# Optimization experiments

Hardware: AMD Instinct MI355X
Metric: run time of the kernel (lower is better)

## Reference

```python
import jax, jax.numpy as jnp
import numpy as np
from functools import partial

B, S, D = 64, 1024, 1024
C = 10  # number of chained GRU steps (self.c)


def setup_inputs() -> dict:
    key = jax.random.key(0)
    ks = jax.random.split(key, 8)
    sc = 1.0 / np.sqrt(D)
    return {
        "feat": jax.random.normal(ks[0], (B, S, D), dtype=jnp.float32),
        "a_w": jax.random.normal(ks[1], (D,), dtype=jnp.float32) * sc,          # Linear(D,1,bias=False)
        "W_ih": jax.random.normal(ks[2], (3 * D, D + 1), dtype=jnp.float32) * sc,  # GRU input weights (r,z,n)
        "W_hh": jax.random.normal(ks[3], (3 * D, D), dtype=jnp.float32) * sc,      # GRU hidden weights (r,z,n)
        "b_ih": jax.random.normal(ks[4], (3 * D,), dtype=jnp.float32) * sc,
        "b_hh": jax.random.normal(ks[5], (3 * D,), dtype=jnp.float32) * sc,
        "W_out": jax.random.normal(ks[6], (1, D), dtype=jnp.float32) * sc,         # out_layer Linear(D,1)
        "b_out": jax.random.normal(ks[7], (1,), dtype=jnp.float32) * sc,
    }


def reference(feat, a_w, W_ih, W_hh, b_ih, b_hh, W_out, b_out):
    # Attention pooling: softmax over sequence dim of a scalar score per frame.
    logits = jnp.einsum("bsd,d->bs", feat, a_w)                 # [B, S]
    w = jax.nn.softmax(logits, axis=1)                           # [B, S]
    pooled = jnp.einsum("bs,bsd->bd", w, feat)                  # [B, D]

    def gru_step(carry, _):
        h, score = carry
        x = jnp.concatenate([pooled, score], axis=-1)            # [B, D+1]
        gi = x @ W_ih.T + b_ih                                   # [B, 3D]
        gh = h @ W_hh.T + b_hh                                   # [B, 3D]
        i_r, i_z, i_n = jnp.split(gi, 3, axis=-1)
        h_r, h_z, h_n = jnp.split(gh, 3, axis=-1)
        r = jax.nn.sigmoid(i_r + h_r)
        z = jax.nn.sigmoid(i_z + h_z)
        n = jnp.tanh(i_n + r * h_n)
        h_new = (1.0 - z) * n + z * h
        score_new = jax.nn.sigmoid(h_new @ W_out.T + b_out)      # [B, 1]
        return (h_new, score_new), score_new

    h0 = jnp.zeros_like(pooled)                                  # GRU hidden starts at zero
    s0 = jnp.zeros((pooled.shape[0], 1), dtype=pooled.dtype)     # zero_score initial chain input
    _, scores = jax.lax.scan(gru_step, (h0, s0), None, length=C)  # scores: [C, B, 1]
    out = jnp.transpose(scores[..., 0], (1, 0))                  # [B, C]
    return out
```

## Files before the change

kernel.cpp:

```cpp
#include <hip/hip_runtime.h>
#include <hip/hip_bf16.h>
#include <math.h>

#define B 64
#define S 1024
#define D 1024
#define C 10
#define TD 3072

typedef __attribute__((ext_vector_type(8))) short s8v;
typedef __attribute__((ext_vector_type(4))) float f4v;
typedef unsigned long long u64;

__device__ __forceinline__ float wave_sum_bc(float v) {
    #pragma unroll
    for (int off = 1; off < 64; off <<= 1) v += __shfl_xor(v, off, 64);
    return v;
}
__device__ __forceinline__ float sigm(float x) { return 1.0f / (1.0f + expf(-x)); }
__device__ __forceinline__ short f2bf(float f) {
    __hip_bfloat16 h = __float2bfloat16(f);
    return *reinterpret_cast<short*>(&h);
}
__device__ __forceinline__ u64 aload64(u64* p) {
    return __hip_atomic_load(p, __ATOMIC_RELAXED, __HIP_MEMORY_SCOPE_AGENT);
}
__device__ __forceinline__ void astore64(u64* p, u64 v) {
    __hip_atomic_store(p, v, __ATOMIC_RELAXED, __HIP_MEMORY_SCOPE_AGENT);
}
__device__ __forceinline__ float aloadf(float* p) {
    return __hip_atomic_load(p, __ATOMIC_RELAXED, __HIP_MEMORY_SCOPE_AGENT);
}
__device__ __forceinline__ void astoref(float* p, float v) {
    __hip_atomic_store(p, v, __ATOMIC_RELAXED, __HIP_MEMORY_SCOPE_AGENT);
}

__global__ __launch_bounds__(256) void k_pre(const float* __restrict__ feat,
        const float* __restrict__ a_w, const float* __restrict__ W_ih,
        const float* __restrict__ W_hh, float* __restrict__ part, float* __restrict__ ml,
        short* __restrict__ BihP, short* __restrict__ BhhP, float* __restrict__ wscore,
        unsigned* __restrict__ bar) {
    __shared__ float sacc[4][1024];
    __shared__ float sml[4][2];
    int n = blockIdx.x, tid = threadIdx.x;

    if (n >= 1024) {
        if (n < 4096) {
            int rel = n - 1024;
            const float* Wsrc = (rel < 1536) ? W_ih : W_hh;
            short* dst = (rel < 1536) ? BihP : BhhP;
            int stride = (rel < 1536) ? (D + 1) : D;
            int rn = (rel < 1536) ? rel : rel - 1536;
            int gid = rn * 256 + tid;
            int fid = gid >> 6, l = gid & 63;
            int s = fid & 31, g = (fid >> 5) % 3, dt = fid / 96;
            int row = g * 1024 + dt * 16 + (l & 15);
            int k0 = s * 32 + ((l >> 4) << 3);
            const float* src = Wsrc + (size_t)row * stride + k0;
            short v[8];
            #pragma unroll
            for (int j = 0; j < 8; ++j) v[j] = f2bf(src[j]);
            short* d = dst + ((size_t)fid * 64 + l) * 8;
            #pragma unroll
            for (int j = 0; j < 8; ++j) d[j] = v[j];
        } else {
            int j = (n - 4096) * 256 + tid;
            wscore[j] = W_ih[(size_t)j * (D + 1) + D];
            if (n == 4096 && tid < 64) bar[tid] = 0u;
        }
        return;
    }

    int ch = n & 15, b = n >> 4;
    int w = tid >> 6, lane = tid & 63;
    float4 aw[4], acc[4];
    #pragma unroll
    for (int r = 0; r < 4; ++r) {
        aw[r] = *reinterpret_cast<const float4*>(&a_w[r * 256 + lane * 4]);
        acc[r] = make_float4(0.f, 0.f, 0.f, 0.f);
    }
    float m = -INFINITY, l = 0.f;
    const float* fb = feat + ((size_t)b * S + ch * 64 + w * 16) * D;
    for (int i = 0; i < 16; ++i) {
        float4 f[4];
        #pragma unroll
        for (int r = 0; r < 4; ++r)
            f[r] = *reinterpret_cast<const float4*>(&fb[(size_t)i * D + r * 256 + lane * 4]);
        float dot = 0.f;
        #pragma unroll
        for (int r = 0; r < 4; ++r)
            dot += f[r].x * aw[r].x + f[r].y * aw[r].y + f[r].z * aw[r].z + f[r].w * aw[r].w;
        dot = wave_sum_bc(dot);
        if (dot <= m) {
            float wg = expf(dot - m);
            l += wg;
            #pragma unroll
            for (int r = 0; r < 4; ++r) {
                acc[r].x += wg * f[r].x; acc[r].y += wg * f[r].y;
                acc[r].z += wg * f[r].z; acc[r].w += wg * f[r].w;
            }
        } else {
            float sc = expf(m - dot);
            l = l * sc + 1.f;
            #pragma unroll
            for (int r = 0; r < 4; ++r) {
                acc[r].x = acc[r].x * sc + f[r].x; acc[r].y = acc[r].y * sc + f[r].y;
                acc[r].z = acc[r].z * sc + f[r].z; acc[r].w = acc[r].w * sc + f[r].w;
            }
            m = dot;
        }
    }
    #pragma unroll
    for (int r = 0; r < 4; ++r)
        *reinterpret_cast<float4*>(&sacc[w][r * 256 + lane * 4]) = acc[r];
    if (lane == 0) { sml[w][0] = m; sml[w][1] = l; }
    __syncthreads();
    float m0 = sml[0][0], m1 = sml[1][0], m2 = sml[2][0], m3 = sml[3][0];
    float mg = fmaxf(fmaxf(m0, m1), fmaxf(m2, m3));
    float s0 = expf(m0 - mg), s1 = expf(m1 - mg), s2 = expf(m2 - mg), s3 = expf(m3 - mg);
    int c = tid * 4;
    float4 a0 = *reinterpret_cast<float4*>(&sacc[0][c]);
    float4 a1 = *reinterpret_cast<float4*>(&sacc[1][c]);
    float4 a2 = *reinterpret_cast<float4*>(&sacc[2][c]);
    float4 a3 = *reinterpret_cast<float4*>(&sacc[3][c]);
    float4 o;
    o.x = s0 * a0.x + s1 * a1.x + s2 * a2.x + s3 * a3.x;
    o.y = s0 * a0.y + s1 * a1.y + s2 * a2.y + s3 * a3.y;
    o.z = s0 * a0.z + s1 * a1.z + s2 * a2.z + s3 * a3.z;
    o.w = s0 * a0.w + s1 * a1.w + s2 * a2.w + s3 * a3.w;
    *reinterpret_cast<float4*>(&part[((size_t)b * 16 + ch) * D + c]) = o;
    if (tid == 0) {
        float lg = s0 * sml[0][1] + s1 * sml[1][1] + s2 * sml[2][1] + s3 * sml[3][1];
        ml[(b * 16 + ch) * 2] = mg;
        ml[(b * 16 + ch) * 2 + 1] = lg;
    }
}

__global__ __launch_bounds__(256) void k_mid(const float* __restrict__ part,
        const float* __restrict__ ml, short* __restrict__ pooledP) {
    int b = blockIdx.x, tid = threadIdx.x;
    float mg = -INFINITY;
    #pragma unroll
    for (int q = 0; q < 16; ++q) mg = fmaxf(mg, ml[(b * 16 + q) * 2]);
    float denom = 0.f, sc[16];
    #pragma unroll
    for (int q = 0; q < 16; ++q) {
        sc[q] = expf(ml[(b * 16 + q) * 2] - mg);
        denom += sc[q] * ml[(b * 16 + q) * 2 + 1];
    }
    float inv = 1.f / denom;
    int c = tid * 4;
    float4 o = make_float4(0.f, 0.f, 0.f, 0.f);
    #pragma unroll
    for (int q = 0; q < 16; ++q) {
        float4 p = *reinterpret_cast<const float4*>(&part[((size_t)b * 16 + q) * D + c]);
        o.x += sc[q] * p.x; o.y += sc[q] * p.y; o.z += sc[q] * p.z; o.w += sc[q] * p.w;
    }
    float ov[4] = {o.x * inv, o.y * inv, o.z * inv, o.w * inv};
    int m = b >> 4;
    #pragma unroll
    for (int j4 = 0; j4 < 4; ++j4) {
        int d = c + j4;
        int s = d >> 5, lane2 = (b & 15) + (((d >> 3) & 3) << 4), jj = d & 7;
        pooledP[(((size_t)m * 32 + s) * 64 + lane2) * 8 + jj] = f2bf(ov[j4]);
    }
}

__global__ __launch_bounds__(512, 2) void k_persist(const s8v* __restrict__ BihP,
        const s8v* __restrict__ BhhP, const short* __restrict__ pooledP,
        u64* hpA, u64* hpB, const float* __restrict__ wscore,
        const float* __restrict__ b_ih, const float* __restrict__ b_hh,
        const float* __restrict__ W_out, const float* __restrict__ b_out,
        float* spart, float* __restrict__ out, unsigned* bar) {
    __shared__ float psum[8][16][49];
    __shared__ float gilds[16][49];
    __shared__ float hl[16][17];
    __shared__ float sredS[16][17];
    __shared__ float sredO[16][17];
    __shared__ unsigned short hbf[16][16];

    int tid = threadIdx.x, w = tid >> 6, l = tid & 63;
    int n = blockIdx.x, xcd = n & 7, slot = n >> 3;
    int dt = xcd * 8 + (slot & 7), bh = slot >> 3;
    int bq0 = bh * 16;
    int lb = tid & 15, c = (tid >> 4) & 15;
    bool epi = (tid < 256);
    int b = bq0 + lb, d = dt * 16 + c;
    unsigned* cnt = &bar[bh * 16];

    float e_bo = b_out[0];
    float e_b0 = 0.f, e_b1 = 0.f, e_b2 = 0.f, e_wo = 0.f;
    float e_w0 = 0.f, e_w1 = 0.f, e_w2 = 0.f;
    if (epi) {
        e_b0 = b_hh[d]; e_b1 = b_hh[D + d]; e_b2 = b_hh[2 * D + d];
        e_wo = W_out[d];
        e_w0 = wscore[d]; e_w1 = wscore[D + d]; e_w2 = wscore[2 * D + d];
    }

    s8v Bw[4][3];
    #pragma unroll
    for (int s8 = 0; s8 < 4; ++s8) {
        int s = w * 4 + s8;
        #pragma unroll
        for (int g = 0; g < 3; ++g)
            Bw[s8][g] = BhhP[((size_t)(dt * 3 + g) * 32 + s) * 64 + l];
    }

    {
        const s8v* Ap = reinterpret_cast<const s8v*>(pooledP);
        f4v acc[3];
        #pragma unroll
        for (int g = 0; g < 3; ++g) acc[g] = (f4v){0.f, 0.f, 0.f, 0.f};
        #pragma unroll
        for (int s8 = 0; s8 < 4; ++s8) {
            int s = w * 4 + s8;
            s8v a = Ap[((size_t)bh * 32 + s) * 64 + l];
            #pragma unroll
            for (int g = 0; g < 3; ++g) {
                s8v bb = BihP[((size_t)(dt * 3 + g) * 32 + s) * 64 + l];
                acc[g] = __builtin_amdgcn_mfma_f32_16x16x32_bf16(a, bb, acc[g], 0, 0, 0);
            }
        }
        #pragma unroll
        for (int g = 0; g < 3; ++g)
            #pragma unroll
            for (int r = 0; r < 4; ++r)
                psum[w][(l >> 4) * 4 + r][g * 16 + (l & 15)] = acc[g][r];
        __syncthreads();
        if (epi) {
            float g3[3];
            #pragma unroll
            for (int g = 0; g < 3; ++g) {
                float v = 0.f;
                #pragma unroll
                for (int ww = 0; ww < 8; ++ww) v += psum[ww][lb][g * 16 + c];
                g3[g] = v;
            }
            float gir = g3[0] + b_ih[d];
            float giz = g3[1] + b_ih[D + d];
            float gin = g3[2] + b_ih[2 * D + d];
            gilds[lb][c] = gir; gilds[lb][16 + c] = giz; gilds[lb][32 + c] = gin;
            float rr = sigm(gir + e_b0);
            float zz = sigm(giz + e_b1);
            float nn = tanhf(gin + rr * e_b2);
            float hnew = (1.f - zz) * nn;
            hl[lb][c] = hnew;
            hbf[lb][c] = (unsigned short)f2bf(hnew);
            sredO[lb][c] = hnew * e_wo;
        }
        __syncthreads();
        if (tid < 64) {
            int lb2 = tid & 15, k4 = tid >> 4;
            u64 v = (u64)hbf[lb2][k4 * 4] | ((u64)hbf[lb2][k4 * 4 + 1] << 16) |
                    ((u64)hbf[lb2][k4 * 4 + 2] << 32) | ((u64)hbf[lb2][k4 * 4 + 3] << 48);
            int q2 = (2 * dt + (k4 >> 1)) & 3;
            int lane2 = lb2 + (q2 << 4);
            size_t idx = (((size_t)bh * 32 + (dt >> 1)) * 64 + lane2) * 2 + (k4 & 1);
            astore64(&hpA[idx], v);
        }
        if (tid < 16) {
            float v = 0.f;
            #pragma unroll
            for (int q = 0; q < 16; ++q) v += sredO[tid][q];
            astoref(&spart[((size_t)0 * B + bq0 + tid) * 64 + dt], v);
        }
        __syncthreads();
        if (tid == 0)
            __hip_atomic_fetch_add(cnt, 1u, __ATOMIC_RELAXED, __HIP_MEMORY_SCOPE_AGENT);
    }

    for (int t = 1; t < C; ++t) {
        if (tid == 0) {
            unsigned tgt = (unsigned)(t * 64);
            while (__hip_atomic_load(cnt, __ATOMIC_RELAXED, __HIP_MEMORY_SCOPE_AGENT) < tgt)
                __builtin_amdgcn_s_sleep(4);
        }
        __syncthreads();
        if (epi) {
            float* sp = &spart[((size_t)(t - 1) * B + b) * 64 + c * 4];
            sredS[lb][c] = aloadf(sp) + aloadf(sp + 1) + aloadf(sp + 2) + aloadf(sp + 3);
        }
        u64* Ain = (t & 1) ? hpA : hpB;
        u64* Aout = (t & 1) ? hpB : hpA;
        f4v acc[3];
        #pragma unroll
        for (int g = 0; g < 3; ++g) acc[g] = (f4v){0.f, 0.f, 0.f, 0.f};
        #pragma unroll
        for (int s8 = 0; s8 < 4; ++s8) {
            int s = w * 4 + s8;
            size_t base = (((size_t)bh * 32 + s) * 64 + l) * 2;
            union { u64 q[2]; s8v v; } au;
            au.q[0] = aload64(&Ain[base]);
            au.q[1] = aload64(&Ain[base + 1]);
            #pragma unroll
            for (int g = 0; g < 3; ++g)
                acc[g] = __builtin_amdgcn_mfma_f32_16x16x32_bf16(au.v, Bw[s8][g], acc[g], 0, 0, 0);
        }
        #pragma unroll
        for (int g = 0; g < 3; ++g)
            #pragma unroll
            for (int r = 0; r < 4; ++r)
                psum[w][(l >> 4) * 4 + r][g * 16 + (l & 15)] = acc[g][r];
        __syncthreads();
        if (epi) {
            float g3[3];
            #pragma unroll
            for (int g = 0; g < 3; ++g) {
                float v = 0.f;
                #pragma unroll
                for (int ww = 0; ww < 8; ++ww) v += psum[ww][lb][g * 16 + c];
                g3[g] = v;
            }
            float ssum = e_bo;
            #pragma unroll
            for (int q = 0; q < 16; ++q) ssum += sredS[lb][q];
            float score = sigm(ssum);
            if (dt == 0 && c == 0) out[b * C + (t - 1)] = score;
            float gir = gilds[lb][c]      + score * e_w0;
            float giz = gilds[lb][16 + c] + score * e_w1;
            float gin = gilds[lb][32 + c] + score * e_w2;
            float rr = sigm(gir + e_b0 + g3[0]);
            float zz = sigm(giz + e_b1 + g3[1]);
            float nn = tanhf(gin + e_b2 + g3[2] + rr * (0.f) + rr * g3[2] * 0.f + 0.f);
            nn = tanhf(gin + rr * (e_b2 + g3[2]));
            float hnew = (1.f - zz) * nn + zz * hl[lb][c];
            hl[lb][c] = hnew;
            hbf[lb][c] = (unsigned short)f2bf(hnew);
            sredO[lb][c] = hnew * e_wo;
        }
        __syncthreads();
        if (tid < 64) {
            int lb2 = tid & 15, k4 = tid >> 4;
            u64 v = (u64)hbf[lb2][k4 * 4] | ((u64)hbf[lb2][k4 * 4 + 1] << 16) |
                    ((u64)hbf[lb2][k4 * 4 + 2] << 32) | ((u64)hbf[lb2][k4 * 4 + 3] << 48);
            int q2 = (2 * dt + (k4 >> 1)) & 3;
            int lane2 = lb2 + (q2 << 4);
            size_t idx = (((size_t)bh * 32 + (dt >> 1)) * 64 + lane2) * 2 + (k4 & 1);
            astore64(&Aout[idx], v);
        }
        if (tid < 16) {
            float v = 0.f;
            #pragma unroll
            for (int q = 0; q < 16; ++q) v += sredO[tid][q];
            astoref(&spart[((size_t)t * B + bq0 + tid) * 64 + dt], v);
        }
        __syncthreads();
        if (tid == 0)
            __hip_atomic_fetch_add(cnt, 1u, __ATOMIC_RELAXED, __HIP_MEMORY_SCOPE_AGENT);
    }

    if (dt == 0) {
        if (tid == 0) {
            unsigned tgt = (unsigned)(C * 64);
            while (__hip_atomic_load(cnt, __ATOMIC_RELAXED, __HIP_MEMORY_SCOPE_AGENT) < tgt)
                __builtin_amdgcn_s_sleep(4);
        }
        __syncthreads();
        if (tid < 16) {
            int bb = bq0 + tid;
            float s = e_bo;
            for (int k = 0; k < 64; ++k)
                s += aloadf(&spart[((size_t)(C - 1) * B + bb) * 64 + k]);
            out[bb * C + (C - 1)] = sigm(s);
        }
    }
}

extern "C" void kernel_launch(void* const* d_in, const int* in_sizes, int n_in,
                              void* d_out, int out_size, void* d_ws, size_t ws_size,
                              hipStream_t stream) {
    const float* feat  = (const float*)d_in[0];
    const float* a_w   = (const float*)d_in[1];
    const float* W_ih  = (const float*)d_in[2];
    const float* W_hh  = (const float*)d_in[3];
    const float* b_ih  = (const float*)d_in[4];
    const float* b_hh  = (const float*)d_in[5];
    const float* W_out = (const float*)d_in[6];
    const float* b_out = (const float*)d_in[7];
    float* out = (float*)d_out;
    float* ws = (float*)d_ws;

    float* part    = ws;
    float* ml      = part + (size_t)B * 16 * D;
    float* spart   = ml + B * 16 * 2;
    float* wscore  = spart + (size_t)C * B * 64;
    short* pooledP = (short*)(wscore + TD);
    short* hpA     = pooledP + (size_t)B * D;
    short* hpB     = hpA + (size_t)B * D;
    short* BihP    = hpB + (size_t)B * D;
    short* BhhP    = BihP + (size_t)D * TD;
    unsigned* bar  = (unsigned*)(BhhP + (size_t)D * TD);

    k_pre<<<dim3(4108), 256, 0, stream>>>(feat, a_w, W_ih, W_hh, part, ml,
                                          BihP, BhhP, wscore, bar);
    k_mid<<<dim3(64), 256, 0, stream>>>(part, ml, pooledP);
    k_persist<<<dim3(256), 512, 0, stream>>>((const s8v*)BihP, (const s8v*)BhhP,
                                             pooledP, (u64*)hpA, (u64*)hpB,
                                             wscore, b_ih, b_hh, W_out, b_out,
                                             spart, out, bar);
}
```

Baseline: 111.9 us.

## Fuse pooling finalize into persistent kernel and split barrier into per-wave counters

Removes the separate k_mid launch by having the first 64 blocks of the persistent kernel compute the softmax-weighted pooled vector and signal it through a global counter that all blocks poll. Replaces the single per-batch-half step counter with eight padded counters, so each wave polls only the counter for the producers whose score partials it reads, dropping a block-wide barrier per step. Also moves the arrival signal to a single wave after an explicit vmcnt wait and hoists the b_ih loads. The gain comes from one fewer kernel launch and finer-grained synchronization, at the cost of more atomic traffic and reliance on relaxed-ordering correctness.

```diff
diff --git a/kernel.cpp b/kernel.cpp
--- a/kernel.cpp
+++ b/kernel.cpp
@@ -28,11 +28,15 @@
 __device__ __forceinline__ void astore64(u64* p, u64 v) {
     __hip_atomic_store(p, v, __ATOMIC_RELAXED, __HIP_MEMORY_SCOPE_AGENT);
 }
-__device__ __forceinline__ float aloadf(float* p) {
-    return __hip_atomic_load(p, __ATOMIC_RELAXED, __HIP_MEMORY_SCOPE_AGENT);
-}
 __device__ __forceinline__ void astoref(float* p, float v) {
     __hip_atomic_store(p, v, __ATOMIC_RELAXED, __HIP_MEMORY_SCOPE_AGENT);
+}
+__device__ __forceinline__ void wave_poll(unsigned* cnt, unsigned tgt, int l) {
+    if (l == 0) {
+        while (__hip_atomic_load(cnt, __ATOMIC_RELAXED, __HIP_MEMORY_SCOPE_AGENT) < tgt)
+            __builtin_amdgcn_s_sleep(1);
+    }
+    asm volatile("" ::: "memory");
 }
 
 __global__ __launch_bounds__(256) void k_pre(const float* __restrict__ feat,
@@ -66,7 +70,10 @@
         } else {
             int j = (n - 4096) * 256 + tid;
             wscore[j] = W_ih[(size_t)j * (D + 1) + D];
-            if (n == 4096 && tid < 64) bar[tid] = 0u;
+            if (n == 4096) {
+                #pragma unroll
+                for (int q = 0; q < 5; ++q) bar[q * 256 + tid] = 0u;
+            }
         }
         return;
     }
@@ -136,46 +143,17 @@
     }
 }
 
-__global__ __launch_bounds__(256) void k_mid(const float* __restrict__ part,
-        const float* __restrict__ ml, short* __restrict__ pooledP) {
-    int b = blockIdx.x, tid = threadIdx.x;
-    float mg = -INFINITY;
-    #pragma unroll
-    for (int q = 0; q < 16; ++q) mg = fmaxf(mg, ml[(b * 16 + q) * 2]);
-    float denom = 0.f, sc[16];
-    #pragma unroll
-    for (int q = 0; q < 16; ++q) {
-        sc[q] = expf(ml[(b * 16 + q) * 2] - mg);
-        denom += sc[q] * ml[(b * 16 + q) * 2 + 1];
-    }
-    float inv = 1.f / denom;
-    int c = tid * 4;
-    float4 o = make_float4(0.f, 0.f, 0.f, 0.f);
-    #pragma unroll
-    for (int q = 0; q < 16; ++q) {
-        float4 p = *reinterpret_cast<const float4*>(&part[((size_t)b * 16 + q) * D + c]);
-        o.x += sc[q] * p.x; o.y += sc[q] * p.y; o.z += sc[q] * p.z; o.w += sc[q] * p.w;
-    }
-    float ov[4] = {o.x * inv, o.y * inv, o.z * inv, o.w * inv};
-    int m = b >> 4;
-    #pragma unroll
-    for (int j4 = 0; j4 < 4; ++j4) {
-        int d = c + j4;
-        int s = d >> 5, lane2 = (b & 15) + (((d >> 3) & 3) << 4), jj = d & 7;
-        pooledP[(((size_t)m * 32 + s) * 64 + lane2) * 8 + jj] = f2bf(ov[j4]);
-    }
-}
-
 __global__ __launch_bounds__(512, 2) void k_persist(const s8v* __restrict__ BihP,
-        const s8v* __restrict__ BhhP, const short* __restrict__ pooledP,
+        const s8v* __restrict__ BhhP, short* pooledP,
         u64* hpA, u64* hpB, const float* __restrict__ wscore,
         const float* __restrict__ b_ih, const float* __restrict__ b_hh,
         const float* __restrict__ W_out, const float* __restrict__ b_out,
+        const float* __restrict__ part, const float* __restrict__ ml,
         float* spart, float* __restrict__ out, unsigned* bar) {
     __shared__ float psum[8][16][49];
     __shared__ float gilds[16][49];
     __shared__ float hl[16][17];
-    __shared__ float sredS[16][17];
+    __shared__ float sredS2[16][33];
     __shared__ float sredO[16][17];
     __shared__ unsigned short hbf[16][16];
 
@@ -183,20 +161,57 @@
     int n = blockIdx.x, xcd = n & 7, slot = n >> 3;
     int dt = xcd * 8 + (slot & 7), bh = slot >> 3;
     int bq0 = bh * 16;
-    int lb = tid & 15, c = (tid >> 4) & 15;
+    int lb = tid & 15, c = (tid >> 4) & 15, c8 = tid >> 4;
     bool epi = (tid < 256);
     int b = bq0 + lb, d = dt * 16 + c;
-    unsigned* cnt = &bar[bh * 16];
+    unsigned* cnt8 = &bar[(bh * 8) * 32];
+    unsigned* cnt_pool = &bar[1024];
+    u64* poolU = (u64*)pooledP;
+
+    if (n < 64 && tid < 256) {
+        int bb = n;
+        float mg = -INFINITY;
+        #pragma unroll
+        for (int q = 0; q < 16; ++q) mg = fmaxf(mg, ml[(bb * 16 + q) * 2]);
+        float denom = 0.f, sc[16];
+        #pragma unroll
+        for (int q = 0; q < 16; ++q) {
+            sc[q] = expf(ml[(bb * 16 + q) * 2] - mg);
+            denom += sc[q] * ml[(bb * 16 + q) * 2 + 1];
+        }
+        float inv = 1.f / denom;
+        int cc = tid * 4;
+        float4 o = make_float4(0.f, 0.f, 0.f, 0.f);
+        #pragma unroll
+        for (int q = 0; q < 16; ++q) {
+            float4 p = *reinterpret_cast<const float4*>(&part[((size_t)bb * 16 + q) * D + cc]);
+            o.x += sc[q] * p.x; o.y += sc[q] * p.y; o.z += sc[q] * p.z; o.w += sc[q] * p.w;
+        }
+        u64 v = (u64)(unsigned short)f2bf(o.x * inv) |
+                ((u64)(unsigned short)f2bf(o.y * inv) << 16) |
+                ((u64)(unsigned short)f2bf(o.z * inv) << 32) |
+                ((u64)(unsigned short)f2bf(o.w * inv) << 48);
+        int lane2 = (bb & 15) + (((cc >> 3) & 3) << 4);
+        size_t idx = (((size_t)(bb >> 4) * 32 + (cc >> 5)) * 64 + lane2) * 2 + ((cc >> 2) & 1);
+        astore64(&poolU[idx], v);
+    }
+    if (n < 64) {
+        __syncthreads();
+        if (tid == 0) {
+            asm volatile("s_waitcnt vmcnt(0)" ::: "memory");
+            __hip_atomic_fetch_add(cnt_pool, 1u, __ATOMIC_RELAXED, __HIP_MEMORY_SCOPE_AGENT);
+        }
+    }
 
     float e_bo = b_out[0];
     float e_b0 = 0.f, e_b1 = 0.f, e_b2 = 0.f, e_wo = 0.f;
-    float e_w0 = 0.f, e_w1 = 0.f, e_w2 = 0.f;
+    float e_w0 = 0.f, e_w1 = 0.f, e_w2 = 0.f, e_i0 = 0.f, e_i1 = 0.f, e_i2 = 0.f;
     if (epi) {
         e_b0 = b_hh[d]; e_b1 = b_hh[D + d]; e_b2 = b_hh[2 * D + d];
         e_wo = W_out[d];
         e_w0 = wscore[d]; e_w1 = wscore[D + d]; e_w2 = wscore[2 * D + d];
-    }
-
+        e_i0 = b_ih[d]; e_i1 = b_ih[D + d]; e_i2 = b_ih[2 * D + d];
+    }
     s8v Bw[4][3];
     #pragma unroll
     for (int s8 = 0; s8 < 4; ++s8) {
@@ -206,19 +221,27 @@
             Bw[s8][g] = BhhP[((size_t)(dt * 3 + g) * 32 + s) * 64 + l];
     }
 
+    if (tid == 0) {
+        while (__hip_atomic_load(cnt_pool, __ATOMIC_RELAXED, __HIP_MEMORY_SCOPE_AGENT) < 64u)
+            __builtin_amdgcn_s_sleep(1);
+    }
+    __syncthreads();
+
     {
-        const s8v* Ap = reinterpret_cast<const s8v*>(pooledP);
         f4v acc[3];
         #pragma unroll
         for (int g = 0; g < 3; ++g) acc[g] = (f4v){0.f, 0.f, 0.f, 0.f};
         #pragma unroll
         for (int s8 = 0; s8 < 4; ++s8) {
             int s = w * 4 + s8;
-            s8v a = Ap[((size_t)bh * 32 + s) * 64 + l];
+            size_t base = (((size_t)bh * 32 + s) * 64 + l) * 2;
+            union { u64 q[2]; s8v v; } au;
+            au.q[0] = aload64(&poolU[base]);
+            au.q[1] = aload64(&poolU[base + 1]);
             #pragma unroll
             for (int g = 0; g < 3; ++g) {
-                s8v bb = BihP[((size_t)(dt * 3 + g) * 32 + s) * 64 + l];
-                acc[g] = __builtin_amdgcn_mfma_f32_16x16x32_bf16(a, bb, acc[g], 0, 0, 0);
+                s8v bb2 = BihP[((size_t)(dt * 3 + g) * 32 + s) * 64 + l];
+                acc[g] = __builtin_amdgcn_mfma_f32_16x16x32_bf16(au.v, bb2, acc[g], 0, 0, 0);
             }
         }
         #pragma unroll
@@ -236,9 +259,7 @@
                 for (int ww = 0; ww < 8; ++ww) v += psum[ww][lb][g * 16 + c];
                 g3[g] = v;
             }
-            float gir = g3[0] + b_ih[d];
-            float giz = g3[1] + b_ih[D + d];
-            float gin = g3[2] + b_ih[2 * D + d];
+            float gir = g3[0] + e_i0, giz = g3[1] + e_i1, gin = g3[2] + e_i2;
             gilds[lb][c] = gir; gilds[lb][16 + c] = giz; gilds[lb][32 + c] = gin;
             float rr = sigm(gir + e_b0);
             float zz = sigm(giz + e_b1);
@@ -255,30 +276,26 @@
                     ((u64)hbf[lb2][k4 * 4 + 2] << 32) | ((u64)hbf[lb2][k4 * 4 + 3] << 48);
             int q2 = (2 * dt + (k4 >> 1)) & 3;
             int lane2 = lb2 + (q2 << 4);
-            size_t idx = (((size_t)bh * 32 + (dt >> 1)) * 64 + lane2) * 2 + (k4 & 1);
-            astore64(&hpA[idx], v);
-        }
-        if (tid < 16) {
-            float v = 0.f;
-            #pragma unroll
-            for (int q = 0; q < 16; ++q) v += sredO[tid][q];
-            astoref(&spart[((size_t)0 * B + bq0 + tid) * 64 + dt], v);
-        }
-        __syncthreads();
-        if (tid == 0)
-            __hip_atomic_fetch_add(cnt, 1u, __ATOMIC_RELAXED, __HIP_MEMORY_SCOPE_AGENT);
+            astore64(&hpA[(((size_t)bh * 32 + (dt >> 1)) * 64 + lane2) * 2 + (k4 & 1)], v);
+            if (tid < 16) {
+                float v2 = 0.f;
+                #pragma unroll
+                for (int q = 0; q < 16; ++q) v2 += sredO[tid][q];
+                astoref(&spart[((size_t)0 * B + bq0 + tid) * 64 + dt], v2);
+            }
+            asm volatile("s_waitcnt vmcnt(0)" ::: "memory");
+            if (tid == 0)
+                __hip_atomic_fetch_add(&cnt8[(dt >> 3) * 32], 1u, __ATOMIC_RELAXED,
+                                       __HIP_MEMORY_SCOPE_AGENT);
+        }
     }
 
     for (int t = 1; t < C; ++t) {
-        if (tid == 0) {
-            unsigned tgt = (unsigned)(t * 64);
-            while (__hip_atomic_load(cnt, __ATOMIC_RELAXED, __HIP_MEMORY_SCOPE_AGENT) < tgt)
-                __builtin_amdgcn_s_sleep(4);
-        }
-        __syncthreads();
-        if (epi) {
-            float* sp = &spart[((size_t)(t - 1) * B + b) * 64 + c * 4];
-            sredS[lb][c] = aloadf(sp) + aloadf(sp + 1) + aloadf(sp + 2) + aloadf(sp + 3);
+        wave_poll(&cnt8[w * 32], (unsigned)(t * 8), l);
+        {
+            union { u64 q; float f[2]; } sv;
+            sv.q = aload64(&((u64*)spart)[((size_t)(t - 1) * B + b) * 32 + c8]);
+            sredS2[lb][c8] = sv.f[0] + sv.f[1];
         }
         u64* Ain = (t & 1) ? hpA : hpB;
         u64* Aout = (t & 1) ? hpB : hpA;
@@ -313,7 +330,7 @@
             }
             float ssum = e_bo;
             #pragma unroll
-            for (int q = 0; q < 16; ++q) ssum += sredS[lb][q];
+            for (int q = 0; q < 32; ++q) ssum += sredS2[lb][q];
             float score = sigm(ssum);
             if (dt == 0 && c == 0) out[b * C + (t - 1)] = score;
             float gir = gilds[lb][c]      + score * e_w0;
@@ -321,8 +338,7 @@
             float gin = gilds[lb][32 + c] + score * e_w2;
             float rr = sigm(gir + e_b0 + g3[0]);
             float zz = sigm(giz + e_b1 + g3[1]);
-            float nn = tanhf(gin + e_b2 + g3[2] + rr * (0.f) + rr * g3[2] * 0.f + 0.f);
-            nn = tanhf(gin + rr * (e_b2 + g3[2]));
+            float nn = tanhf(gin + rr * (e_b2 + g3[2]));
             float hnew = (1.f - zz) * nn + zz * hl[lb][c];
             hl[lb][c] = hnew;
             hbf[lb][c] = (unsigned short)f2bf(hnew);
@@ -335,32 +351,31 @@
                     ((u64)hbf[lb2][k4 * 4 + 2] << 32) | ((u64)hbf[lb2][k4 * 4 + 3] << 48);
             int q2 = (2 * dt + (k4 >> 1)) & 3;
             int lane2 = lb2 + (q2 << 4);
-            size_t idx = (((size_t)bh * 32 + (dt >> 1)) * 64 + lane2) * 2 + (k4 & 1);
-            astore64(&Aout[idx], v);
-        }
-        if (tid < 16) {
-            float v = 0.f;
-            #pragma unroll
-            for (int q = 0; q < 16; ++q) v += sredO[tid][q];
-            astoref(&spart[((size_t)t * B + bq0 + tid) * 64 + dt], v);
-        }
-        __syncthreads();
-        if (tid == 0)
-            __hip_atomic_fetch_add(cnt, 1u, __ATOMIC_RELAXED, __HIP_MEMORY_SCOPE_AGENT);
+            astore64(&Aout[(((size_t)bh * 32 + (dt >> 1)) * 64 + lane2) * 2 + (k4 & 1)], v);
+            if (tid < 16) {
+                float v2 = 0.f;
+                #pragma unroll
+                for (int q = 0; q < 16; ++q) v2 += sredO[tid][q];
+                astoref(&spart[((size_t)t * B + bq0 + tid) * 64 + dt], v2);
+            }
+            asm volatile("s_waitcnt vmcnt(0)" ::: "memory");
+            if (tid == 0)
+                __hip_atomic_fetch_add(&cnt8[(dt >> 3) * 32], 1u, __ATOMIC_RELAXED,
+                                       __HIP_MEMORY_SCOPE_AGENT);
+        }
     }
 
     if (dt == 0) {
-        if (tid == 0) {
-            unsigned tgt = (unsigned)(C * 64);
-            while (__hip_atomic_load(cnt, __ATOMIC_RELAXED, __HIP_MEMORY_SCOPE_AGENT) < tgt)
-                __builtin_amdgcn_s_sleep(4);
-        }
+        wave_poll(&cnt8[w * 32], (unsigned)(C * 8), l);
         __syncthreads();
         if (tid < 16) {
             int bb = bq0 + tid;
             float s = e_bo;
-            for (int k = 0; k < 64; ++k)
-                s += aloadf(&spart[((size_t)(C - 1) * B + bb) * 64 + k]);
+            for (int k = 0; k < 64; ++k) {
+                float pv = __hip_atomic_load(&spart[((size_t)(C - 1) * B + bb) * 64 + k],
+                                             __ATOMIC_RELAXED, __HIP_MEMORY_SCOPE_AGENT);
+                s += pv;
+            }
             out[bb * C + (C - 1)] = sigm(s);
         }
     }
@@ -393,9 +408,8 @@
 
     k_pre<<<dim3(4108), 256, 0, stream>>>(feat, a_w, W_ih, W_hh, part, ml,
                                           BihP, BhhP, wscore, bar);
-    k_mid<<<dim3(64), 256, 0, stream>>>(part, ml, pooledP);
     k_persist<<<dim3(256), 512, 0, stream>>>((const s8v*)BihP, (const s8v*)BhhP,
                                              pooledP, (u64*)hpA, (u64*)hpB,
                                              wscore, b_ih, b_hh, W_out, b_out,
-                                             spart, out, bar);
-}
+                                             part, ml, spart, out, bar);
+}
```

Result: no change. 110.9 us (-0.9%).
